# Kernel tuning notes

Hardware: AMD Instinct MI355X
Metric: run time of the kernel (lower is better)

## Reference

```python
import jax, jax.numpy as jnp
import numpy as np

N = 50000
E = 800000
F_IN = 128
HID = 128
NCLS = 40


def setup_inputs() -> dict:
    key = jax.random.key(0)
    ks = jax.random.split(key, 12)
    def glorot(k, fan_in, fan_out):
        s = jnp.sqrt(6.0 / (fan_in + fan_out))
        return jax.random.uniform(k, (fan_in, fan_out), jnp.float32, -s, s)
    x = jax.random.normal(ks[0], (N, F_IN), jnp.float32)
    edge_index = jax.random.randint(ks[1], (2, E), 0, N, jnp.int64)
    W1 = glorot(ks[2], F_IN, HID); b1 = jnp.zeros((HID,), jnp.float32)
    W2 = glorot(ks[3], HID, HID);  b2 = jnp.zeros((HID,), jnp.float32)
    W3 = glorot(ks[4], HID, HID);  b3 = jnp.zeros((HID,), jnp.float32)
    Wc = glorot(ks[5], HID, NCLS)
    bc = jnp.zeros((NCLS,), jnp.float32)
    return {"x": x, "edge_index": edge_index, "W1": W1, "b1": b1,
            "W2": W2, "b2": b2, "W3": W3, "b3": b3, "Wc": Wc, "bc": bc}


def _gcn_conv(h, src, dst, norm, W, b):
    # GCNConv: linear transform, then normalized scatter-add aggregation
    h = h @ W                              # [N, out]
    msg = h[src] * norm[:, None]           # [E+N, out] gathered + scaled
    out = jax.ops.segment_sum(msg, dst, num_segments=N)
    return out + b


def reference(x, edge_index, W1, b1, W2, b2, W3, b3, Wc, bc):
    # add self-loops (PyG GCNConv default) and compute symmetric norm once
    loop = jnp.arange(N, dtype=edge_index.dtype)
    src = jnp.concatenate([edge_index[0], loop])
    dst = jnp.concatenate([edge_index[1], loop])
    deg = jax.ops.segment_sum(jnp.ones_like(dst, dtype=x.dtype), dst, num_segments=N)
    dinv = jax.lax.rsqrt(deg)              # deg >= 1 due to self-loops
    norm = dinv[src] * dinv[dst]           # [E+N]

    h = jax.nn.relu(_gcn_conv(x, src, dst, norm, W1, b1))
    h = jax.nn.relu(_gcn_conv(h, src, dst, norm, W2, b2))
    h = jax.nn.relu(_gcn_conv(h, src, dst, norm, W3, b3))
    out = h @ Wc + bc
    return (out, h)
```

## Files before the change

kernel.cpp:

```cpp
#include <hip/hip_runtime.h>
#include <hip/hip_fp16.h>


#define FEAT 128

typedef _Float16 half_t;
typedef _Float16 f16x8 __attribute__((ext_vector_type(8)));
typedef float f32x16 __attribute__((ext_vector_type(16)));
typedef unsigned int u32x4 __attribute__((ext_vector_type(4)));


__global__ __launch_bounds__(256) void k_prep(const float* __restrict__ W1,
                                              const float* __restrict__ W2,
                                              const float* __restrict__ W3,
                                              half_t* __restrict__ Wt1,
                                              half_t* __restrict__ Wt2,
                                              half_t* __restrict__ Wt3,
                                              int* __restrict__ deg, int N) {
  int idx = blockIdx.x * 256 + threadIdx.x;
  if (idx < N) deg[idx] = 0;
  if (idx < 3 * 16384) {
    int which = idx >> 14;
    int i = idx & 16383;
    int k = i >> 7, n = i & 127;
    const float* W = (which == 0) ? W1 : (which == 1) ? W2 : W3;
    half_t* Wt = (which == 0) ? Wt1 : (which == 1) ? Wt2 : Wt3;
    Wt[n * 128 + k] = (half_t)W[i];
  }
}


__global__ __launch_bounds__(256) void k_count_rank(const int* __restrict__ dst,
                                                    int* __restrict__ deg,
                                                    int* __restrict__ rank, int E) {
  int e = blockIdx.x * 256 + threadIdx.x;
  if (e < E) {
    int r = atomicAdd(&deg[dst[e]], 1);
    __builtin_nontemporal_store(r, &rank[e]);
  }
}

__global__ __launch_bounds__(256) void k_scanA(const int* __restrict__ deg,
                                               int* __restrict__ partial, int N) {
  __shared__ int s[256];
  int t = threadIdx.x;
  int i = blockIdx.x * 256 + t;
  s[t] = (i < N) ? deg[i] : 0;
  __syncthreads();
  for (int off = 128; off > 0; off >>= 1) {
    if (t < off) s[t] += s[t + off];
    __syncthreads();
  }
  if (t == 0) partial[blockIdx.x] = s[0];
}

__global__ __launch_bounds__(256) void k_scanC2(const int* __restrict__ deg,
                                                const int* __restrict__ partial,
                                                int* __restrict__ offsets,
                                                float* __restrict__ dinv, int N) {
  __shared__ int s[256];
  int t = threadIdx.x;
  int i = blockIdx.x * 256 + t;
  int base = 0;
  for (int j = 0; j < blockIdx.x; ++j) base += partial[j];
  int v = (i < N) ? deg[i] : 0;
  s[t] = v;
  __syncthreads();
  for (int off = 1; off < 256; off <<= 1) {
    int x = (t >= off) ? s[t - off] : 0;
    __syncthreads();
    s[t] += x;
    __syncthreads();
  }
  if (i < N) {
    offsets[i] = base + s[t] - v;
    dinv[i] = rsqrtf((float)(v + 1));
    if (i == N - 1) offsets[N] = base + s[t];
  }
}

__global__ __launch_bounds__(256) void k_place(const int* __restrict__ src,
                                               const int* __restrict__ dst,
                                               const int* __restrict__ offsets,
                                               const int* __restrict__ rank,
                                               int* __restrict__ col, int E) {
  int e = blockIdx.x * 256 + threadIdx.x;
  if (e < E) {
    int r = __builtin_nontemporal_load(&rank[e]);
    col[offsets[dst[e]] + r] = src[e];
  }
}

template <int SRC_FP32>
__global__ __launch_bounds__(256) void k_gemm_mfma(const void* __restrict__ Asrc,
                                                   const half_t* __restrict__ Wt,
                                                   const float* __restrict__ dinv,
                                                   half_t* __restrict__ T,
                                                   int nrows) {
  __shared__ char lds[49152];
  char* sA = lds;
  char* sW = lds + 32768;
  int t = threadIdx.x;
  int rowBase = blockIdx.x * 128;
  int rowsHere = min(128, nrows - rowBase);

  if (SRC_FP32) {
    const float* Af = (const float*)Asrc;
    #pragma unroll
    for (int i = 0; i < 8; ++i) {
      int lin = t + i * 256;
      int r = lin >> 4, c = lin & 15;
      f16x8 h = {};
      if (r < rowsHere) {
        const float4* p = (const float4*)(Af + (size_t)(rowBase + r) * FEAT + c * 8);
        float4 v0 = p[0], v1 = p[1];
        h[0] = (half_t)v0.x; h[1] = (half_t)v0.y; h[2] = (half_t)v0.z; h[3] = (half_t)v0.w;
        h[4] = (half_t)v1.x; h[5] = (half_t)v1.y; h[6] = (half_t)v1.z; h[7] = (half_t)v1.w;
      }
      *(f16x8*)(sA + r * 256 + ((c * 16) ^ ((r & 15) << 4))) = h;
    }
  } else {
    const char* Ah = (const char*)Asrc;
    #pragma unroll
    for (int i = 0; i < 8; ++i) {
      int lin = t + i * 256;
      int r = lin >> 4, c = lin & 15;
      float4 v = {};
      if (r < rowsHere) v = *(const float4*)(Ah + (size_t)(rowBase + r) * 256 + c * 16);
      *(float4*)(sA + r * 256 + ((c * 16) ^ ((r & 15) << 4))) = v;
    }
  }

  int wv = t >> 6;
  int l = t & 63;
  int l31 = l & 31;
  int lhi = l >> 5;
  int sw = (l31 & 15) << 4;

  f32x16 acc[4] = {};

  #pragma unroll
  for (int ch = 0; ch < 2; ++ch) {
    if (ch) __syncthreads();
    #pragma unroll
    for (int i = 0; i < 4; ++i) {
      int lin = t + i * 256;
      int r = lin >> 4, c = lin & 15;
      *(float4*)(sW + r * 256 + ((c * 16) ^ ((r & 15) << 4))) =
          *(const float4*)((const char*)Wt + (ch * 64 + r) * 256 + c * 16);
    }
    __syncthreads();
    #pragma unroll
    for (int step = 0; step < 8; ++step) {
      int ko = (step * 32 + lhi * 16) ^ sw;
      f16x8 a  = *(const f16x8*)(sA + (wv * 32 + l31) * 256 + ko);
      f16x8 b0 = *(const f16x8*)(sW + (l31) * 256 + ko);
      f16x8 b1 = *(const f16x8*)(sW + (32 + l31) * 256 + ko);
      acc[2 * ch + 0] = __builtin_amdgcn_mfma_f32_32x32x16_f16(a, b0, acc[2 * ch + 0], 0, 0, 0);
      acc[2 * ch + 1] = __builtin_amdgcn_mfma_f32_32x32x16_f16(a, b1, acc[2 * ch + 1], 0, 0, 0);
    }
  }

  #pragma unroll
  for (int j = 0; j < 16; ++j) {
    int rloc = wv * 32 + (j & 3) + 8 * (j >> 2) + 4 * lhi;
    if (rloc < rowsHere) {
      int grow = rowBase + rloc;
      float d = dinv[grow];
      #pragma unroll
      for (int n = 0; n < 4; ++n) {
        T[(size_t)grow * FEAT + n * 32 + l31] = (half_t)(acc[n][j] * d);
      }
    }
  }
}


__device__ __forceinline__ void acc8(float* a, u32x4 v) {
  unsigned w0 = v[0], w1 = v[1], w2 = v[2], w3 = v[3];
  __half2 p0 = *(__half2*)&w0, p1 = *(__half2*)&w1;
  __half2 p2 = *(__half2*)&w2, p3 = *(__half2*)&w3;
  a[0] += __half2float(p0.x); a[1] += __half2float(p0.y);
  a[2] += __half2float(p1.x); a[3] += __half2float(p1.y);
  a[4] += __half2float(p2.x); a[5] += __half2float(p2.y);
  a[6] += __half2float(p3.x); a[7] += __half2float(p3.y);
}

__device__ __forceinline__ void gather_node(const u32x4* __restrict__ T8,
                                            const int* __restrict__ offsets,
                                            const int* __restrict__ col,
                                            int node, int q, float* a) {
  u32x4 sv = T8[(size_t)node * 16 + q];
  {
    unsigned w0 = sv[0], w1 = sv[1], w2 = sv[2], w3 = sv[3];
    __half2 p0 = *(__half2*)&w0, p1 = *(__half2*)&w1;
    __half2 p2 = *(__half2*)&w2, p3 = *(__half2*)&w3;
    a[0] = __half2float(p0.x); a[1] = __half2float(p0.y);
    a[2] = __half2float(p1.x); a[3] = __half2float(p1.y);
    a[4] = __half2float(p2.x); a[5] = __half2float(p2.y);
    a[6] = __half2float(p3.x); a[7] = __half2float(p3.y);
  }
  int e0 = offsets[node], e1 = offsets[node + 1];
  int e = e0;
  for (; e + 8 <= e1; e += 8) {
    int s[8];
    u32x4 v[8];
    #pragma unroll
    for (int u = 0; u < 8; ++u) s[u] = __builtin_nontemporal_load(&col[e + u]);
    #pragma unroll
    for (int u = 0; u < 8; ++u) v[u] = T8[(size_t)s[u] * 16 + q];
    #pragma unroll
    for (int u = 0; u < 8; ++u) acc8(a, v[u]);
  }
  for (; e < e1; ++e) {
    int s = __builtin_nontemporal_load(&col[e]);
    acc8(a, T8[(size_t)s * 16 + q]);
  }
}

template <int OUTF>
__global__ __launch_bounds__(256) void k_aggregate(const u32x4* __restrict__ T8,
                                                   const int* __restrict__ offsets,
                                                   const int* __restrict__ col,
                                                   const float* __restrict__ dinv,
                                                   const float* __restrict__ bias,
                                                   u32x4* __restrict__ outH,
                                                   float4* __restrict__ outF,
                                                   int N) {
  int t = threadIdx.x;
  int node = blockIdx.x * 16 + (t >> 4);
  int q = t & 15;
  if (node >= N) return;

  float a[8];
  gather_node(T8, offsets, col, node, q, a);

  float di = dinv[node];
  const float4* b4 = (const float4*)bias;
  float4 bA = b4[2 * q], bB = b4[2 * q + 1];
  float o0 = fmaxf(di * a[0] + bA.x, 0.f);
  float o1 = fmaxf(di * a[1] + bA.y, 0.f);
  float o2 = fmaxf(di * a[2] + bA.z, 0.f);
  float o3 = fmaxf(di * a[3] + bA.w, 0.f);
  float o4 = fmaxf(di * a[4] + bB.x, 0.f);
  float o5 = fmaxf(di * a[5] + bB.y, 0.f);
  float o6 = fmaxf(di * a[6] + bB.z, 0.f);
  float o7 = fmaxf(di * a[7] + bB.w, 0.f);

  if (OUTF) {
    outF[(size_t)node * 32 + 2 * q] = make_float4(o0, o1, o2, o3);
    outF[(size_t)node * 32 + 2 * q + 1] = make_float4(o4, o5, o6, o7);
  } else {
    __half2 h0 = __floats2half2_rn(o0, o1), h1 = __floats2half2_rn(o2, o3);
    __half2 h2 = __floats2half2_rn(o4, o5), h3 = __floats2half2_rn(o6, o7);
    u32x4 o;
    o[0] = *(unsigned*)&h0; o[1] = *(unsigned*)&h1;
    o[2] = *(unsigned*)&h2; o[3] = *(unsigned*)&h3;
    __builtin_nontemporal_store(o, &outH[(size_t)node * 16 + q]);
  }
}

__global__ __launch_bounds__(256) void k_classifier(const float* __restrict__ h,
                                                    const float* __restrict__ Wc,
                                                    const float* __restrict__ bc,
                                                    float* __restrict__ out, int N) {
  __shared__ float sh[64 * 132];
  __shared__ float sWt[40 * 130];
  int t = threadIdx.x;
  int nodeBase = blockIdx.x * 64;
  int nodesHere = min(64, N - nodeBase);

  for (int i = t; i < FEAT * 40; i += 256) {
    int k = i / 40, c = i - k * 40;
    sWt[c * 130 + k] = Wc[i];
  }
  {
    const float4* H4 = (const float4*)(h + (size_t)nodeBase * FEAT);
    #pragma unroll
    for (int i = 0; i < 8; ++i) {
      int lin = t + i * 256;
      int r = lin >> 5, kc = lin & 31;
      float4 v = make_float4(0.f, 0.f, 0.f, 0.f);
      if (r < nodesHere) v = H4[lin];
      *(float4*)&sh[r * 132 + kc * 4] = v;
    }
  }
  __syncthreads();

  int n0 = (t >> 3) * 2;
  int cg = (t & 7) * 5;
  float acc0[5], acc1[5];
  #pragma unroll
  for (int j = 0; j < 5; ++j) { acc0[j] = bc[cg + j]; acc1[j] = acc0[j]; }

  #pragma unroll 4
  for (int k4 = 0; k4 < 32; ++k4) {
    float4 h0 = *(const float4*)&sh[n0 * 132 + k4 * 4];
    float4 h1 = *(const float4*)&sh[(n0 + 1) * 132 + k4 * 4];
    #pragma unroll
    for (int j = 0; j < 5; ++j) {
      float4 w = *(const float4*)&sWt[(cg + j) * 130 + k4 * 4];
      acc0[j] += h0.x * w.x + h0.y * w.y + h0.z * w.z + h0.w * w.w;
      acc1[j] += h1.x * w.x + h1.y * w.y + h1.z * w.z + h1.w * w.w;
    }
  }

  if (n0 < nodesHere) {
    float* o = out + (size_t)(nodeBase + n0) * 40 + cg;
    #pragma unroll
    for (int j = 0; j < 5; ++j) __builtin_nontemporal_store(acc0[j], &o[j]);
  }
  if (n0 + 1 < nodesHere) {
    float* o = out + (size_t)(nodeBase + n0 + 1) * 40 + cg;
    #pragma unroll
    for (int j = 0; j < 5; ++j) __builtin_nontemporal_store(acc1[j], &o[j]);
  }
}


extern "C" void kernel_launch(void* const* d_in, const int* in_sizes, int n_in,
                              void* d_out, int out_size, void* d_ws, size_t ws_size,
                              hipStream_t stream) {
  const float* x    = (const float*)d_in[0];
  const int*   edge = (const int*)d_in[1];
  const float* W1   = (const float*)d_in[2];
  const float* b1   = (const float*)d_in[3];
  const float* W2   = (const float*)d_in[4];
  const float* b2   = (const float*)d_in[5];
  const float* W3   = (const float*)d_in[6];
  const float* b3   = (const float*)d_in[7];
  const float* Wc   = (const float*)d_in[8];
  const float* bc   = (const float*)d_in[9];

  int N = in_sizes[0] / FEAT;
  int E = in_sizes[1] / 2;

  float* out  = (float*)d_out;
  float* hOut = out + (size_t)N * 40;

  size_t o = 0;
  char* wsb = (char*)d_ws;
  auto take = [&](size_t bytes) -> void* {
    void* p = wsb + o;
    o += (bytes + 255) & ~(size_t)255;
    return p;
  };
  float*   dinv    = (float*)take((size_t)N * 4);
  int*     deg     = (int*)take((size_t)N * 4);
  int*     rank    = (int*)take((size_t)E * 4);
  int*     partial = (int*)take(256 * 4);
  int*     offsets = (int*)take(((size_t)N + 8) * 4);
  int*     col     = (int*)take((size_t)E * 4);
  half_t*  T2h     = (half_t*)take((size_t)N * FEAT * 2);
  half_t*  Bh      = (half_t*)take((size_t)N * FEAT * 2);
  half_t*  Wt1     = (half_t*)take(16384 * 2);
  half_t*  Wt2     = (half_t*)take(16384 * 2);
  half_t*  Wt3     = (half_t*)take(16384 * 2);

  const int* e_src = edge;
  const int* e_dst = edge + E;

  int nblk = (N + 255) / 256;
  int eblk = (E + 255) / 256;

  k_prep<<<nblk, 256, 0, stream>>>(W1, W2, W3, Wt1, Wt2, Wt3, deg, N);
  k_count_rank<<<eblk, 256, 0, stream>>>(e_dst, deg, rank, E);
  k_scanA<<<nblk, 256, 0, stream>>>(deg, partial, N);
  k_scanC2<<<nblk, 256, 0, stream>>>(deg, partial, offsets, dinv, N);
  k_place<<<eblk, 256, 0, stream>>>(e_src, e_dst, offsets, rank, col, E);

  int gblk = (N + 127) / 128;
  int ablk = (N + 15) / 16;
  u32x4* T8 = (u32x4*)T2h;
  k_gemm_mfma<1><<<gblk, 256, 0, stream>>>(x, Wt1, dinv, T2h, N);
  k_aggregate<0><<<ablk, 256, 0, stream>>>(T8, offsets, col, dinv, b1,
                                           (u32x4*)Bh, nullptr, N);
  k_gemm_mfma<0><<<gblk, 256, 0, stream>>>(Bh, Wt2, dinv, T2h, N);
  k_aggregate<0><<<ablk, 256, 0, stream>>>(T8, offsets, col, dinv, b2,
                                           (u32x4*)Bh, nullptr, N);
  k_gemm_mfma<0><<<gblk, 256, 0, stream>>>(Bh, Wt3, dinv, T2h, N);
  k_aggregate<1><<<ablk, 256, 0, stream>>>(T8, offsets, col, dinv, b3,
                                           nullptr, (float4*)hOut, N);
  k_classifier<<<(N + 63) / 64, 256, 0, stream>>>(hOut, Wc, bc, out, N);
}
```

Baseline: 253.7 us.

## Sort aggregation nodes by degree, load full weight tile once, drop nontemporal hints

Builds a descending-degree permutation of nodes using a 256-bin histogram, a scan and atomic placement. The aggregation kernels then walk nodes in that order, so the 16-lane groups in a block handle similar edge counts and divergence and tail imbalance shrink. The GEMM now loads the whole 128x128 weight tile into 64KB of LDS at once, removing a barrier and a reload. Nontemporal loads and stores become regular ones so they stay in cache. The cost is an extra kernel launch, some atomics, scattered output writes, and possibly lower occupancy from the larger LDS footprint.

Result: slower. 494.5 us (+95.0%).

```diff
diff --git a/kernel.cpp b/kernel.cpp
--- a/kernel.cpp
+++ b/kernel.cpp
@@ -16,9 +16,12 @@
                                               half_t* __restrict__ Wt1,
                                               half_t* __restrict__ Wt2,
                                               half_t* __restrict__ Wt3,
-                                              int* __restrict__ deg, int N) {
+                                              int* __restrict__ deg,
+                                              int* __restrict__ hist,
+                                              int* __restrict__ histCnt, int N) {
   int idx = blockIdx.x * 256 + threadIdx.x;
   if (idx < N) deg[idx] = 0;
+  if (idx < 256) { hist[idx] = 0; histCnt[idx] = 0; }
   if (idx < 3 * 16384) {
     int which = idx >> 14;
     int i = idx & 16383;
@@ -41,11 +44,14 @@
 }
 
 __global__ __launch_bounds__(256) void k_scanA(const int* __restrict__ deg,
-                                               int* __restrict__ partial, int N) {
+                                               int* __restrict__ partial,
+                                               int* __restrict__ hist, int N) {
   __shared__ int s[256];
   int t = threadIdx.x;
   int i = blockIdx.x * 256 + t;
-  s[t] = (i < N) ? deg[i] : 0;
+  int v = (i < N) ? deg[i] : 0;
+  s[t] = v;
+  if (i < N) atomicAdd(&hist[255 - min(v, 255)], 1);
   __syncthreads();
   for (int off = 128; off > 0; off >>= 1) {
     if (t < off) s[t] += s[t + off];
@@ -54,10 +60,29 @@
   if (t == 0) partial[blockIdx.x] = s[0];
 }
 
+__global__ __launch_bounds__(256) void k_histscan(const int* __restrict__ hist,
+                                                  int* __restrict__ histBase) {
+  __shared__ int s[256];
+  int t = threadIdx.x;
+  int v = hist[t];
+  s[t] = v;
+  __syncthreads();
+  for (int off = 1; off < 256; off <<= 1) {
+    int x = (t >= off) ? s[t - off] : 0;
+    __syncthreads();
+    s[t] += x;
+    __syncthreads();
+  }
+  histBase[t] = s[t] - v;
+}
+
 __global__ __launch_bounds__(256) void k_scanC2(const int* __restrict__ deg,
                                                 const int* __restrict__ partial,
                                                 int* __restrict__ offsets,
-                                                float* __restrict__ dinv, int N) {
+                                                float* __restrict__ dinv,
+                                                const int* __restrict__ histBase,
+                                                int* __restrict__ histCnt,
+                                                int* __restrict__ perm, int N) {
   __shared__ int s[256];
   int t = threadIdx.x;
   int i = blockIdx.x * 256 + t;
@@ -76,6 +101,9 @@
     offsets[i] = base + s[t] - v;
     dinv[i] = rsqrtf((float)(v + 1));
     if (i == N - 1) offsets[N] = base + s[t];
+    int b = 255 - min(v, 255);
+    int pos = histBase[b] + atomicAdd(&histCnt[b], 1);
+    perm[pos] = i;
   }
 }
 
@@ -97,13 +125,20 @@
                                                    const float* __restrict__ dinv,
                                                    half_t* __restrict__ T,
                                                    int nrows) {
-  __shared__ char lds[49152];
+  __shared__ char lds[65536];
   char* sA = lds;
   char* sW = lds + 32768;
   int t = threadIdx.x;
   int rowBase = blockIdx.x * 128;
   int rowsHere = min(128, nrows - rowBase);
 
+  #pragma unroll
+  for (int i = 0; i < 8; ++i) {
+    int lin = t + i * 256;
+    int r = lin >> 4, c = lin & 15;
+    *(float4*)(sW + r * 256 + ((c * 16) ^ ((r & 15) << 4))) =
+        *(const float4*)((const char*)Wt + r * 256 + c * 16);
+  }
   if (SRC_FP32) {
     const float* Af = (const float*)Asrc;
     #pragma unroll
@@ -130,6 +165,7 @@
       *(float4*)(sA + r * 256 + ((c * 16) ^ ((r & 15) << 4))) = v;
     }
   }
+  __syncthreads();
 
   int wv = t >> 6;
   int l = t & 63;
@@ -140,25 +176,17 @@
   f32x16 acc[4] = {};
 
   #pragma unroll
-  for (int ch = 0; ch < 2; ++ch) {
-    if (ch) __syncthreads();
-    #pragma unroll
-    for (int i = 0; i < 4; ++i) {
-      int lin = t + i * 256;
-      int r = lin >> 4, c = lin & 15;
-      *(float4*)(sW + r * 256 + ((c * 16) ^ ((r & 15) << 4))) =
-          *(const float4*)((const char*)Wt + (ch * 64 + r) * 256 + c * 16);
-    }
-    __syncthreads();
-    #pragma unroll
-    for (int step = 0; step < 8; ++step) {
-      int ko = (step * 32 + lhi * 16) ^ sw;
-      f16x8 a  = *(const f16x8*)(sA + (wv * 32 + l31) * 256 + ko);
-      f16x8 b0 = *(const f16x8*)(sW + (l31) * 256 + ko);
-      f16x8 b1 = *(const f16x8*)(sW + (32 + l31) * 256 + ko);
-      acc[2 * ch + 0] = __builtin_amdgcn_mfma_f32_32x32x16_f16(a, b0, acc[2 * ch + 0], 0, 0, 0);
-      acc[2 * ch + 1] = __builtin_amdgcn_mfma_f32_32x32x16_f16(a, b1, acc[2 * ch + 1], 0, 0, 0);
-    }
+  for (int step = 0; step < 8; ++step) {
+    int ko = (step * 32 + lhi * 16) ^ sw;
+    f16x8 a  = *(const f16x8*)(sA + (wv * 32 + l31) * 256 + ko);
+    f16x8 b0 = *(const f16x8*)(sW + (l31) * 256 + ko);
+    f16x8 b1 = *(const f16x8*)(sW + (32 + l31) * 256 + ko);
+    f16x8 b2 = *(const f16x8*)(sW + (64 + l31) * 256 + ko);
+    f16x8 b3 = *(const f16x8*)(sW + (96 + l31) * 256 + ko);
+    acc[0] = __builtin_amdgcn_mfma_f32_32x32x16_f16(a, b0, acc[0], 0, 0, 0);
+    acc[1] = __builtin_amdgcn_mfma_f32_32x32x16_f16(a, b1, acc[1], 0, 0, 0);
+    acc[2] = __builtin_amdgcn_mfma_f32_32x32x16_f16(a, b2, acc[2], 0, 0, 0);
+    acc[3] = __builtin_amdgcn_mfma_f32_32x32x16_f16(a, b3, acc[3], 0, 0, 0);
   }
 
   #pragma unroll
@@ -206,31 +234,30 @@
     int s[8];
     u32x4 v[8];
     #pragma unroll
-    for (int u = 0; u < 8; ++u) s[u] = __builtin_nontemporal_load(&col[e + u]);
+    for (int u = 0; u < 8; ++u) s[u] = col[e + u];
     #pragma unroll
     for (int u = 0; u < 8; ++u) v[u] = T8[(size_t)s[u] * 16 + q];
     #pragma unroll
     for (int u = 0; u < 8; ++u) acc8(a, v[u]);
   }
-  for (; e < e1; ++e) {
-    int s = __builtin_nontemporal_load(&col[e]);
-    acc8(a, T8[(size_t)s * 16 + q]);
-  }
+  for (; e < e1; ++e) acc8(a, T8[(size_t)col[e] * 16 + q]);
 }
 
 template <int OUTF>
 __global__ __launch_bounds__(256) void k_aggregate(const u32x4* __restrict__ T8,
                                                    const int* __restrict__ offsets,
                                                    const int* __restrict__ col,
+                                                   const int* __restrict__ perm,
                                                    const float* __restrict__ dinv,
                                                    const float* __restrict__ bias,
                                                    u32x4* __restrict__ outH,
                                                    float4* __restrict__ outF,
                                                    int N) {
   int t = threadIdx.x;
-  int node = blockIdx.x * 16 + (t >> 4);
+  int gid = blockIdx.x * 16 + (t >> 4);
   int q = t & 15;
-  if (node >= N) return;
+  if (gid >= N) return;
+  int node = perm[gid];
 
   float a[8];
   gather_node(T8, offsets, col, node, q, a);
@@ -256,7 +283,7 @@
     u32x4 o;
     o[0] = *(unsigned*)&h0; o[1] = *(unsigned*)&h1;
     o[2] = *(unsigned*)&h2; o[3] = *(unsigned*)&h3;
-    __builtin_nontemporal_store(o, &outH[(size_t)node * 16 + q]);
+    outH[(size_t)node * 16 + q] = o;
   }
 }
 
@@ -308,12 +335,12 @@
   if (n0 < nodesHere) {
     float* o = out + (size_t)(nodeBase + n0) * 40 + cg;
     #pragma unroll
-    for (int j = 0; j < 5; ++j) __builtin_nontemporal_store(acc0[j], &o[j]);
+    for (int j = 0; j < 5; ++j) o[j] = acc0[j];
   }
   if (n0 + 1 < nodesHere) {
     float* o = out + (size_t)(nodeBase + n0 + 1) * 40 + cg;
     #pragma unroll
-    for (int j = 0; j < 5; ++j) __builtin_nontemporal_store(acc1[j], &o[j]);
+    for (int j = 0; j < 5; ++j) o[j] = acc1[j];
   }
 }
 
@@ -345,17 +372,21 @@
     o += (bytes + 255) & ~(size_t)255;
     return p;
   };
-  float*   dinv    = (float*)take((size_t)N * 4);
-  int*     deg     = (int*)take((size_t)N * 4);
-  int*     rank    = (int*)take((size_t)E * 4);
-  int*     partial = (int*)take(256 * 4);
-  int*     offsets = (int*)take(((size_t)N + 8) * 4);
-  int*     col     = (int*)take((size_t)E * 4);
-  half_t*  T2h     = (half_t*)take((size_t)N * FEAT * 2);
-  half_t*  Bh      = (half_t*)take((size_t)N * FEAT * 2);
-  half_t*  Wt1     = (half_t*)take(16384 * 2);
-  half_t*  Wt2     = (half_t*)take(16384 * 2);
-  half_t*  Wt3     = (half_t*)take(16384 * 2);
+  float*   dinv     = (float*)take((size_t)N * 4);
+  int*     deg      = (int*)take((size_t)N * 4);
+  int*     rank     = (int*)take((size_t)E * 4);
+  int*     partial  = (int*)take(256 * 4);
+  int*     hist     = (int*)take(256 * 4);
+  int*     histBase = (int*)take(256 * 4);
+  int*     histCnt  = (int*)take(256 * 4);
+  int*     offsets  = (int*)take(((size_t)N + 8) * 4);
+  int*     perm     = (int*)take((size_t)N * 4);
+  int*     col      = (int*)take((size_t)E * 4);
+  half_t*  T2h      = (half_t*)take((size_t)N * FEAT * 2);
+  half_t*  Bh       = (half_t*)take((size_t)N * FEAT * 2);
+  half_t*  Wt1      = (half_t*)take(16384 * 2);
+  half_t*  Wt2      = (half_t*)take(16384 * 2);
+  half_t*  Wt3      = (half_t*)take(16384 * 2);
 
   const int* e_src = edge;
   const int* e_dst = edge + E;
@@ -363,23 +394,25 @@
   int nblk = (N + 255) / 256;
   int eblk = (E + 255) / 256;
 
-  k_prep<<<nblk, 256, 0, stream>>>(W1, W2, W3, Wt1, Wt2, Wt3, deg, N);
+  k_prep<<<nblk, 256, 0, stream>>>(W1, W2, W3, Wt1, Wt2, Wt3, deg, hist, histCnt, N);
   k_count_rank<<<eblk, 256, 0, stream>>>(e_dst, deg, rank, E);
-  k_scanA<<<nblk, 256, 0, stream>>>(deg, partial, N);
-  k_scanC2<<<nblk, 256, 0, stream>>>(deg, partial, offsets, dinv, N);
+  k_scanA<<<nblk, 256, 0, stream>>>(deg, partial, hist, N);
+  k_histscan<<<1, 256, 0, stream>>>(hist, histBase);
+  k_scanC2<<<nblk, 256, 0, stream>>>(deg, partial, offsets, dinv, histBase,
+                                     histCnt, perm, N);
   k_place<<<eblk, 256, 0, stream>>>(e_src, e_dst, offsets, rank, col, E);
 
   int gblk = (N + 127) / 128;
   int ablk = (N + 15) / 16;
   u32x4* T8 = (u32x4*)T2h;
   k_gemm_mfma<1><<<gblk, 256, 0, stream>>>(x, Wt1, dinv, T2h, N);
-  k_aggregate<0><<<ablk, 256, 0, stream>>>(T8, offsets, col, dinv, b1,
+  k_aggregate<0><<<ablk, 256, 0, stream>>>(T8, offsets, col, perm, dinv, b1,
                                            (u32x4*)Bh, nullptr, N);
   k_gemm_mfma<0><<<gblk, 256, 0, stream>>>(Bh, Wt2, dinv, T2h, N);
-  k_aggregate<0><<<ablk, 256, 0, stream>>>(T8, offsets, col, dinv, b2,
+  k_aggregate<0><<<ablk, 256, 0, stream>>>(T8, offsets, col, perm, dinv, b2,
                                            (u32x4*)Bh, nullptr, N);
   k_gemm_mfma<0><<<gblk, 256, 0, stream>>>(Bh, Wt3, dinv, T2h, N);
-  k_aggregate<1><<<ablk, 256, 0, stream>>>(T8, offsets, col, dinv, b3,
+  k_aggregate<1><<<ablk, 256, 0, stream>>>(T8, offsets, col, perm, dinv, b3,
                                            nullptr, (float4*)hOut, N);
   k_classifier<<<(N + 63) / 64, 256, 0, stream>>>(hOut, Wc, bc, out, N);
 }
```
